# Kernel optimization log

Hardware: AMD Instinct MI355X
Metric: run time of the kernel (lower is better)

Reference implementation:

```python
import jax, jax.numpy as jnp
import numpy as np

BN_EPS = 1e-5

def _conv1x1(x, W, b):
    # x: (B,C,H,W), W: (O,C) -> (B,O,H,W)
    return jnp.einsum('oc,bchw->bohw', W, x) + b[None, :, None, None]

def setup_inputs() -> dict:
    key = jax.random.key(0)
    ks = jax.random.split(key, 6)
    B, C, H, W = 4, 256, 64, 64
    cq = C // 8
    x  = jax.random.normal(ks[0], (B, C, H, W), jnp.float32)
    Wq = jax.random.normal(ks[1], (cq, C), jnp.float32) * (1.0 / np.sqrt(C))
    Wk = jax.random.normal(ks[2], (cq, C), jnp.float32) * (1.0 / np.sqrt(C))
    Wv = jax.random.normal(ks[3], (C, C), jnp.float32) * (1.0 / np.sqrt(C))
    Wo = jax.random.normal(ks[4], (C, C, 3, 3), jnp.float32) * (1.0 / np.sqrt(C * 9))
    return {
        'x': x,
        'Wq': Wq, 'bq': jnp.zeros((cq,), jnp.float32),
        'Wk': Wk, 'bk': jnp.zeros((cq,), jnp.float32),
        'Wv': Wv, 'bv': jnp.zeros((C,), jnp.float32),
        'Wo': Wo, 'bo': jnp.zeros((C,), jnp.float32),
        'bn_gamma': jnp.ones((C,), jnp.float32),
        'bn_beta':  jnp.zeros((C,), jnp.float32),
        'bn_mean':  jnp.zeros((C,), jnp.float32),
        'bn_var':   jnp.ones((C,), jnp.float32),
    }

def reference(x, Wq, bq, Wk, bk, Wv, bv, Wo, bo, bn_gamma, bn_beta, bn_mean, bn_var):
    B, C, H, W = x.shape
    cq = Wq.shape[0]
    N = H * W
    q = _conv1x1(x, Wq, bq).reshape(B, cq, N)   # (B,cq,N)
    k = _conv1x1(x, Wk, bk).reshape(B, cq, N)   # (B,cq,N)
    v = _conv1x1(x, Wv, bv).reshape(B, C, N)    # (B,C,N)
    scale = cq ** (-0.5)
    attn = jnp.einsum('bcn,bcm->bnm', q, k) * scale   # (B,N,N)
    attn = jax.nn.softmax(attn, axis=-1)
    out = jnp.einsum('bnm,bcm->bcn', attn, v).reshape(B, C, H, W)
    # conv_output: 3x3 conv + BN (inference stats) + ReLU
    out = jax.lax.conv_general_dilated(
        out, Wo, window_strides=(1, 1), padding=((1, 1), (1, 1)),
        dimension_numbers=('NCHW', 'OIHW', 'NCHW')) + bo[None, :, None, None]
    inv = bn_gamma * jax.lax.rsqrt(bn_var + BN_EPS)
    out = out * inv[None, :, None, None] + (bn_beta - bn_mean * inv)[None, :, None, None]
    out = jax.nn.relu(out)
    return out + x
```

## Files before the change

### kernel.cpp

```cpp
#include <hip/hip_runtime.h>
#include <hip/hip_bf16.h>
#include <math.h>

#define N_TOK 4096

typedef __attribute__((ext_vector_type(8))) short short8;
typedef __attribute__((ext_vector_type(4))) float f32x4;

#define MFMA16(a, b, c) __builtin_amdgcn_mfma_f32_16x16x32_bf16(a, b, c, 0, 0, 0)

__device__ inline unsigned pack_bf16x2(float a, float b) {
    __hip_bfloat16 ha = __float2bfloat16(a), hb = __float2bfloat16(b);
    unsigned short ua = *(unsigned short*)&ha, ub = *(unsigned short*)&hb;
    return (unsigned)ua | ((unsigned)ub << 16);
}

__device__ inline float bf2f(unsigned short u) {
    unsigned v = ((unsigned)u) << 16;
    union { unsigned u; float f; } cv; cv.u = v; return cv.f;
}

__device__ inline int swz4(int h, int row) { return (h ^ row ^ (row >> 2)) & 3; }

#define SCK 0.25506974748975505f

__global__ __launch_bounds__(256) void w_prep_kernel(
    const float* __restrict__ Wo, const float* __restrict__ Wq,
    const float* __restrict__ Wk, const float* __restrict__ Wv,
    __hip_bfloat16* __restrict__ Wt, __hip_bfloat16* __restrict__ Wqk,
    __hip_bfloat16* __restrict__ Wvb)
{
    int blk = blockIdx.x, t = threadIdx.x;
    if (blk < 256) {
        const float* src = &Wo[(size_t)(blk * 256 + t) * 9];
#pragma unroll
        for (int tap = 0; tap < 9; ++tap)
            Wt[(size_t)(tap * 256 + blk) * 256 + t] = __float2bfloat16(src[tap]);
    } else if (blk < 260) {
        int r0 = (blk - 256) * 64;
        for (int r = r0; r < r0 + 64; ++r)
            Wvb[r * 256 + t] = __float2bfloat16(Wv[r * 256 + t]);
    } else {
        for (int r = 0; r < 32; ++r) {
            Wqk[r * 256 + t]        = __float2bfloat16(Wq[r * 256 + t] * SCK);
            Wqk[(r + 32) * 256 + t] = __float2bfloat16(Wk[r * 256 + t]);
        }
    }
}

__global__ __launch_bounds__(256) void qkv_kernel(
    const float* __restrict__ x,
    const __hip_bfloat16* __restrict__ Wqk, const __hip_bfloat16* __restrict__ Wvb,
    const float* __restrict__ bq, const float* __restrict__ bk,
    const float* __restrict__ bv,
    __hip_bfloat16* __restrict__ qg, __hip_bfloat16* __restrict__ kg,
    __hip_bfloat16* __restrict__ vg)
{
    __shared__ __hip_bfloat16 tl[64][72];
    int blk = blockIdx.x;
    int b = blk >> 6, n0 = (blk & 63) * 64;
    int t = threadIdx.x, w = t >> 6, lane = t & 63;
    int l15 = lane & 15, l4 = lane >> 4;
    int n = n0 + w * 16 + l15;

    f32x4 zf = {0.f, 0.f, 0.f, 0.f};
    f32x4 aqk[4], av[16];
#pragma unroll
    for (int m = 0; m < 4; ++m) aqk[m] = zf;
#pragma unroll
    for (int m = 0; m < 16; ++m) av[m] = zf;

    int cr = t >> 4, part = t & 15;

    for (int cc = 0; cc < 256; cc += 64) {
        __syncthreads();
#pragma unroll
        for (int rep = 0; rep < 4; ++rep) {
            int c = rep * 16 + cr;
            float4 v4 = *(const float4*)&x[((size_t)(b * 256 + cc + c)) * N_TOK + n0 + part * 4];
            tl[part * 4 + 0][c] = __float2bfloat16(v4.x);
            tl[part * 4 + 1][c] = __float2bfloat16(v4.y);
            tl[part * 4 + 2][c] = __float2bfloat16(v4.z);
            tl[part * 4 + 3][c] = __float2bfloat16(v4.w);
        }
        __syncthreads();
#pragma unroll
        for (int kk = 0; kk < 2; ++kk) {
            int k0 = cc + kk * 32;
            short8 bfr = *(const short8*)&tl[w * 16 + l15][kk * 32 + l4 * 8];
#pragma unroll
            for (int m = 0; m < 4; ++m) {
                short8 af = *(const short8*)&Wqk[(size_t)(m * 16 + l15) * 256 + k0 + l4 * 8];
                aqk[m] = MFMA16(af, bfr, aqk[m]);
            }
#pragma unroll
            for (int m = 0; m < 16; ++m) {
                short8 af = *(const short8*)&Wvb[(size_t)(m * 16 + l15) * 256 + k0 + l4 * 8];
                av[m] = MFMA16(af, bfr, av[m]);
            }
        }
    }

    f32x4 bq0 = *(const f32x4*)&bq[l4 * 4];
    f32x4 bq1 = *(const f32x4*)&bq[16 + l4 * 4];
    f32x4 bk0 = *(const f32x4*)&bk[l4 * 4];
    f32x4 bk1 = *(const f32x4*)&bk[16 + l4 * 4];
    size_t obase = (size_t)(b * N_TOK + n) * 32;
    uint2 u;
    u.x = pack_bf16x2(aqk[0][0] + bq0[0] * SCK, aqk[0][1] + bq0[1] * SCK);
    u.y = pack_bf16x2(aqk[0][2] + bq0[2] * SCK, aqk[0][3] + bq0[3] * SCK);
    *(uint2*)&qg[obase + l4 * 4] = u;
    u.x = pack_bf16x2(aqk[1][0] + bq1[0] * SCK, aqk[1][1] + bq1[1] * SCK);
    u.y = pack_bf16x2(aqk[1][2] + bq1[2] * SCK, aqk[1][3] + bq1[3] * SCK);
    *(uint2*)&qg[obase + 16 + l4 * 4] = u;
    u.x = pack_bf16x2(aqk[2][0] + bk0[0], aqk[2][1] + bk0[1]);
    u.y = pack_bf16x2(aqk[2][2] + bk0[2], aqk[2][3] + bk0[3]);
    *(uint2*)&kg[obase + l4 * 4] = u;
    u.x = pack_bf16x2(aqk[3][0] + bk1[0], aqk[3][1] + bk1[1]);
    u.y = pack_bf16x2(aqk[3][2] + bk1[2], aqk[3][3] + bk1[3]);
    *(uint2*)&kg[obase + 16 + l4 * 4] = u;

#pragma unroll
    for (int m = 0; m < 16; ++m) {
        int cb = m * 16 + l4 * 4;
        f32x4 bvv = *(const f32x4*)&bv[cb];
#pragma unroll
        for (int r = 0; r < 4; ++r)
            vg[((size_t)(b * 256 + cb + r)) * N_TOK + n] = __float2bfloat16(av[m][r] + bvv[r]);
    }
}

__global__ __launch_bounds__(256, 2) void flash_kernel(
    const __hip_bfloat16* __restrict__ qg, const __hip_bfloat16* __restrict__ kg,
    const __hip_bfloat16* __restrict__ vg,
    __hip_bfloat16* __restrict__ ph0, __hip_bfloat16* __restrict__ ph1,
    float* __restrict__ Lh)
{
    __shared__ __hip_bfloat16 v_lds[2][128 * 64];
    __shared__ __hip_bfloat16 k_lds[2][64 * 32];
    __shared__ __hip_bfloat16 p_lds[4][32 * 64];

    int blk = blockIdx.x;
    int work = (blk & 7) * 64 + (blk >> 3);
    int g = work >> 6;
    int kh = g >> 2, cs = (g >> 1) & 1, bl = g & 1;
    int rem = work & 63;
    int b = ((rem >> 5) << 1) | bl;
    int qgp = rem & 31;
    int t = threadIdx.x, w = t >> 6, lane = t & 63;
    int l15 = lane & 15, l4 = lane >> 4;
    int qw = qgp * 128 + w * 32;

    short8 qf[2];
#pragma unroll
    for (int qs = 0; qs < 2; ++qs)
        qf[qs] = *(const short8*)&qg[((size_t)(b * N_TOK + qw + qs * 16 + l15)) * 32 + l4 * 8];

    f32x4 zf = {0.f, 0.f, 0.f, 0.f};
    f32x4 acc[2][8];
#pragma unroll
    for (int qs = 0; qs < 2; ++qs)
#pragma unroll
        for (int ct = 0; ct < 8; ++ct) acc[qs][ct] = zf;
    float Lr[2] = {0.f, 0.f};

    int vc  = t >> 1;
    int kb4 = (t & 1) * 4;
    int kr  = t >> 2;
    int kch = t & 3;

    const __hip_bfloat16* vrow  = &vg[((size_t)(b * 256 + cs * 128 + vc)) * N_TOK + kh * 2048];
    const __hip_bfloat16* kbase = &kg[((size_t)(b * N_TOK + kh * 2048)) * 32];

    uint4 vp[4], kp;

#pragma unroll
    for (int j = 0; j < 4; ++j)
        vp[j] = *(const uint4*)&vrow[(kb4 + j) * 8];
    kp = *(const uint4*)&kbase[kr * 32 + kch * 8];
#pragma unroll
    for (int j = 0; j < 4; ++j)
        *(uint4*)&v_lds[0][vc * 64 + (((2 * (kb4 + j)) ^ (vc & 14)) << 2)] = vp[j];
    *(uint4*)&k_lds[0][kr * 32 + swz4(kch, kr) * 8] = kp;
    __syncthreads();

    int buf = 0;
    for (int it = 0; it < 32; ++it) {
        int nm0 = it * 64 + 64;
        bool more = (it < 31);
        if (more) {
#pragma unroll
            for (int j = 0; j < 4; ++j)
                vp[j] = *(const uint4*)&vrow[nm0 + (kb4 + j) * 8];
            kp = *(const uint4*)&kbase[(size_t)(nm0 + kr) * 32 + kch * 8];
        }

        short8 kf[4];
#pragma unroll
        for (int kt = 0; kt < 4; ++kt) {
            int row = kt * 16 + l15;
            kf[kt] = *(const short8*)&k_lds[buf][row * 32 + swz4(l4, row) * 8];
        }
        f32x4 sf[2][4];
#pragma unroll
        for (int qs = 0; qs < 2; ++qs)
#pragma unroll
            for (int kt = 0; kt < 4; ++kt)
                sf[qs][kt] = MFMA16(kf[kt], qf[qs], zf);

#pragma unroll
        for (int qs = 0; qs < 2; ++qs) {
            int prow = qs * 16 + l15;
#pragma unroll
            for (int kt = 0; kt < 4; ++kt) {
                float p0 = exp2f(sf[qs][kt][0]);
                float p1 = exp2f(sf[qs][kt][1]);
                float p2 = exp2f(sf[qs][kt][2]);
                float p3 = exp2f(sf[qs][kt][3]);
                Lr[qs] += (p0 + p1) + (p2 + p3);
                uint2 u;
                u.x = pack_bf16x2(p0, p1);
                u.y = pack_bf16x2(p2, p3);
                *(uint2*)&p_lds[w][prow * 64 + (((kt * 4 + l4) ^ (l15 & 14)) << 2)] = u;
            }
        }

#pragma unroll
        for (int ks = 0; ks < 2; ++ks) {
            short8 pb[2];
#pragma unroll
            for (int qs = 0; qs < 2; ++qs)
                pb[qs] = *(const short8*)&p_lds[w][(qs * 16 + l15) * 64 +
                         (((ks * 8 + l4 * 2) ^ (l15 & 14)) << 2)];
#pragma unroll
            for (int ct = 0; ct < 8; ++ct) {
                int cr = ct * 16 + l15;
                short8 vf = *(const short8*)&v_lds[buf][cr * 64 +
                           (((ks * 8 + l4 * 2) ^ (cr & 14)) << 2)];
                acc[0][ct] = MFMA16(vf, pb[0], acc[0][ct]);
                acc[1][ct] = MFMA16(vf, pb[1], acc[1][ct]);
            }
        }

        if (more) {
#pragma unroll
            for (int j = 0; j < 4; ++j)
                *(uint4*)&v_lds[buf ^ 1][vc * 64 + (((2 * (kb4 + j)) ^ (vc & 14)) << 2)] = vp[j];
            *(uint4*)&k_lds[buf ^ 1][kr * 32 + swz4(kch, kr) * 8] = kp;
            buf ^= 1;
        }
        __syncthreads();
    }

#pragma unroll
    for (int qs = 0; qs < 2; ++qs) {
        float L = Lr[qs];
        L += __shfl_xor(L, 16);
        L += __shfl_xor(L, 32);
        int nq = qw + qs * 16 + l15;
        if (cs == 0 && l4 == 0)
            Lh[kh * 16384 + b * 4096 + nq] = L;
        __hip_bfloat16* pdst = kh ? ph1 : ph0;
        size_t pix = (size_t)(b * N_TOK + nq);
#pragma unroll
        for (int ct = 0; ct < 8; ++ct) {
            int cl = cs * 128 + ct * 16 + l4 * 4;
            uint2 u;
            u.x = pack_bf16x2(acc[qs][ct][0], acc[qs][ct][1]);
            u.y = pack_bf16x2(acc[qs][ct][2], acc[qs][ct][3]);
            *(uint2*)&pdst[pix * 256 + cl] = u;
        }
    }
}

__global__ __launch_bounds__(256) void conv_mfma_kernel(
    const __hip_bfloat16* __restrict__ ph0, const __hip_bfloat16* __restrict__ ph1,
    const float* __restrict__ Lh, const __hip_bfloat16* __restrict__ Wt,
    const float* __restrict__ bo,  const float* __restrict__ gamma,
    const float* __restrict__ beta, const float* __restrict__ mean,
    const float* __restrict__ var, const float* __restrict__ x,
    float* __restrict__ out)
{
    __shared__ __hip_bfloat16 in_lds[180 * 32];
    __shared__ __hip_bfloat16 wt_lds[9 * 64 * 32];

    int blk = blockIdx.x;
    int sp = blk & 31, ob = (blk >> 5) & 3, b = blk >> 7;
    int y0 = (sp >> 2) * 8, x0 = (sp & 3) * 16;
    int o0 = ob * 64;
    int t = threadIdx.x;
    int w = t >> 6, lane = t & 63;
    int l15 = lane & 15, l4 = lane >> 4;

    f32x4 zf = {0.f, 0.f, 0.f, 0.f};
    f32x4 acc[4][2];
#pragma unroll
    for (int m = 0; m < 4; ++m)
#pragma unroll
        for (int n = 0; n < 2; ++n) acc[m][n] = zf;

    for (int cc = 0; cc < 256; cc += 32) {
        __syncthreads();
        for (int jj = t; jj < 720; jj += 256) {
            int pix = jj >> 2, h = jj & 3;
            int iy = pix / 18, ix = pix - iy * 18;
            int gy = y0 - 1 + iy, gx = x0 - 1 + ix;
            uint4 val = {0u, 0u, 0u, 0u};
            if (gy >= 0 && gy < 64 && gx >= 0 && gx < 64) {
                int bn = b * 4096 + gy * 64 + gx;
                float inv = 1.f / (Lh[bn] + Lh[16384 + bn]);
                size_t e = (size_t)bn * 256 + cc + h * 8;
                uint4 a  = *(const uint4*)&ph0[e];
                uint4 b4 = *(const uint4*)&ph1[e];
                const unsigned* ap = (const unsigned*)&a;
                const unsigned* bp = (const unsigned*)&b4;
                unsigned* vpn = (unsigned*)&val;
#pragma unroll
                for (int j = 0; j < 4; ++j) {
                    float lo = (bf2f((unsigned short)(ap[j] & 0xffff)) +
                                bf2f((unsigned short)(bp[j] & 0xffff))) * inv;
                    float hi = (bf2f((unsigned short)(ap[j] >> 16)) +
                                bf2f((unsigned short)(bp[j] >> 16))) * inv;
                    vpn[j] = pack_bf16x2(lo, hi);
                }
            }
            *(uint4*)&in_lds[pix * 32 + swz4(h, pix) * 8] = val;
        }
        for (int jj = t; jj < 2304; jj += 256) {
            int tap = jj >> 8, rem = jj & 255;
            int o = rem >> 2, h = rem & 3;
            uint4 wv = *(const uint4*)&Wt[((size_t)(tap * 256 + o0 + o)) * 256 + cc + h * 8];
            *(uint4*)&wt_lds[tap * 2048 + o * 32 + swz4(h, o) * 8] = wv;
        }
        __syncthreads();

#pragma unroll
        for (int ky = 0; ky < 3; ++ky) {
#pragma unroll
            for (int kx = 0; kx < 3; ++kx) {
                int tap = ky * 3 + kx;
                short8 af[4];
#pragma unroll
                for (int m = 0; m < 4; ++m) {
                    int orow = m * 16 + l15;
                    af[m] = *(const short8*)&wt_lds[tap * 2048 + orow * 32 + swz4(l4, orow) * 8];
                }
#pragma unroll
                for (int ntw = 0; ntw < 2; ++ntw) {
                    int yy = w * 2 + ntw;
                    int p = (yy + ky) * 18 + kx + l15;
                    short8 bfr = *(const short8*)&in_lds[p * 32 + swz4(l4, p) * 8];
#pragma unroll
                    for (int m = 0; m < 4; ++m)
                        acc[m][ntw] = MFMA16(af[m], bfr, acc[m][ntw]);
                }
            }
        }
    }

#pragma unroll
    for (int m = 0; m < 4; ++m) {
#pragma unroll
        for (int r = 0; r < 4; ++r) {
            int oc = o0 + m * 16 + l4 * 4 + r;
            float inv = gamma[oc] * rsqrtf(var[oc] + 1e-5f);
            float sh  = (bo[oc] - mean[oc]) * inv + beta[oc];
#pragma unroll
            for (int ntw = 0; ntw < 2; ++ntw) {
                int gy = y0 + w * 2 + ntw, gx = x0 + l15;
                size_t idx = (size_t)(b * 256 + oc) * 4096 + (size_t)gy * 64 + gx;
                float yv = acc[m][ntw][r] * inv + sh;
                yv = fmaxf(yv, 0.f);
                out[idx] = yv + x[idx];
            }
        }
    }
}

extern "C" void kernel_launch(void* const* d_in, const int* in_sizes, int n_in,
                              void* d_out, int out_size, void* d_ws, size_t ws_size,
                              hipStream_t stream)
{
    const float* x  = (const float*)d_in[0];
    const float* Wq = (const float*)d_in[1];
    const float* bq = (const float*)d_in[2];
    const float* Wk = (const float*)d_in[3];
    const float* bk = (const float*)d_in[4];
    const float* Wv = (const float*)d_in[5];
    const float* bv = (const float*)d_in[6];
    const float* Wo = (const float*)d_in[7];
    const float* bo = (const float*)d_in[8];
    const float* gm = (const float*)d_in[9];
    const float* bt = (const float*)d_in[10];
    const float* mn = (const float*)d_in[11];
    const float* vr = (const float*)d_in[12];
    float* out = (float*)d_out;

    char* wsb = (char*)d_ws;
    __hip_bfloat16* qg  = (__hip_bfloat16*)(wsb);
    __hip_bfloat16* kg  = (__hip_bfloat16*)(wsb + (1u  << 20));
    __hip_bfloat16* vg  = (__hip_bfloat16*)(wsb + (2u  << 20));
    __hip_bfloat16* ph1 = (__hip_bfloat16*)(wsb + (10u << 20));
    __hip_bfloat16* Wt  = (__hip_bfloat16*)(wsb + (18u << 20));
    __hip_bfloat16* ph0 = (__hip_bfloat16*)(wsb + (20u << 20));
    __hip_bfloat16* Wqk = (__hip_bfloat16*)(wsb + (28u << 20));
    __hip_bfloat16* Wvb = (__hip_bfloat16*)(wsb + (28u << 20) + 65536);
    float*          Lh  = (float*)(wsb + (28u << 20) + 262144);

    w_prep_kernel  <<<261,  256, 0, stream>>>(Wo, Wq, Wk, Wv, Wt, Wqk, Wvb);
    qkv_kernel     <<<256,  256, 0, stream>>>(x, Wqk, Wvb, bq, bk, bv, qg, kg, vg);
    flash_kernel   <<<512,  256, 0, stream>>>(qg, kg, vg, ph0, ph1, Lh);
    conv_mfma_kernel<<<512, 256, 0, stream>>>(ph0, ph1, Lh, Wt, bo, gm, bt, mn, vr, x, out);
}
```

Measured before the change: 155.2 us.

## Split QKV projection across waves by output rows and double grid size

The QKV projection kernel now processes 32 tokens per block instead of 64 and launches 512 blocks. Each wave pair splits the 320 output rows into two groups of 10 MFMA tiles, which cuts per-wave accumulator registers from 20 tiles to 10 and doubles block-level parallelism. The flash kernel loop is also unrolled by 2 so the double-buffer index becomes a compile-time value. The trade-off is that the x tile is loaded and converted once per 32 tokens, so weight reads from cache are repeated across twice as many blocks.

New measurement: 187.5 us. 20.8% more time.

```diff
diff --git a/kernel.cpp b/kernel.cpp
--- a/kernel.cpp
+++ b/kernel.cpp
@@ -56,77 +56,90 @@
     __hip_bfloat16* __restrict__ qg, __hip_bfloat16* __restrict__ kg,
     __hip_bfloat16* __restrict__ vg)
 {
-    __shared__ __hip_bfloat16 tl[64][72];
+    __shared__ __hip_bfloat16 tl[32][72];
     int blk = blockIdx.x;
-    int b = blk >> 6, n0 = (blk & 63) * 64;
+    int b = blk >> 7, n0 = (blk & 127) * 32;
     int t = threadIdx.x, w = t >> 6, lane = t & 63;
     int l15 = lane & 15, l4 = lane >> 4;
-    int n = n0 + w * 16 + l15;
+    int ns = w & 1, mg = w >> 1;
+    int n = n0 + ns * 16 + l15;
+
+    const __hip_bfloat16* wrow[10];
+#pragma unroll
+    for (int mi = 0; mi < 10; ++mi) {
+        int row = mg ? ((6 + mi) * 16 + l15)
+                     : (mi < 4 ? (mi * 16 + l15) : 0);
+        const __hip_bfloat16* base = mg ? Wvb : (mi < 4 ? Wqk : Wvb);
+        if (!mg && mi >= 4) row = (mi - 4) * 16 + l15;
+        wrow[mi] = &base[(size_t)row * 256];
+    }
 
     f32x4 zf = {0.f, 0.f, 0.f, 0.f};
-    f32x4 aqk[4], av[16];
-#pragma unroll
-    for (int m = 0; m < 4; ++m) aqk[m] = zf;
-#pragma unroll
-    for (int m = 0; m < 16; ++m) av[m] = zf;
-
-    int cr = t >> 4, part = t & 15;
+    f32x4 acc[10];
+#pragma unroll
+    for (int m = 0; m < 10; ++m) acc[m] = zf;
 
     for (int cc = 0; cc < 256; cc += 64) {
         __syncthreads();
 #pragma unroll
-        for (int rep = 0; rep < 4; ++rep) {
-            int c = rep * 16 + cr;
-            float4 v4 = *(const float4*)&x[((size_t)(b * 256 + cc + c)) * N_TOK + n0 + part * 4];
-            tl[part * 4 + 0][c] = __float2bfloat16(v4.x);
-            tl[part * 4 + 1][c] = __float2bfloat16(v4.y);
-            tl[part * 4 + 2][c] = __float2bfloat16(v4.z);
-            tl[part * 4 + 3][c] = __float2bfloat16(v4.w);
+        for (int rep = 0; rep < 2; ++rep) {
+            int c = rep * 32 + (t >> 3);
+            int n4 = (t & 7) * 4;
+            float4 v4 = *(const float4*)&x[((size_t)(b * 256 + cc + c)) * N_TOK + n0 + n4];
+            tl[n4 + 0][c] = __float2bfloat16(v4.x);
+            tl[n4 + 1][c] = __float2bfloat16(v4.y);
+            tl[n4 + 2][c] = __float2bfloat16(v4.z);
+            tl[n4 + 3][c] = __float2bfloat16(v4.w);
         }
         __syncthreads();
 #pragma unroll
         for (int kk = 0; kk < 2; ++kk) {
             int k0 = cc + kk * 32;
-            short8 bfr = *(const short8*)&tl[w * 16 + l15][kk * 32 + l4 * 8];
-#pragma unroll
-            for (int m = 0; m < 4; ++m) {
-                short8 af = *(const short8*)&Wqk[(size_t)(m * 16 + l15) * 256 + k0 + l4 * 8];
-                aqk[m] = MFMA16(af, bfr, aqk[m]);
-            }
-#pragma unroll
-            for (int m = 0; m < 16; ++m) {
-                short8 af = *(const short8*)&Wvb[(size_t)(m * 16 + l15) * 256 + k0 + l4 * 8];
-                av[m] = MFMA16(af, bfr, av[m]);
-            }
-        }
-    }
-
-    f32x4 bq0 = *(const f32x4*)&bq[l4 * 4];
-    f32x4 bq1 = *(const f32x4*)&bq[16 + l4 * 4];
-    f32x4 bk0 = *(const f32x4*)&bk[l4 * 4];
-    f32x4 bk1 = *(const f32x4*)&bk[16 + l4 * 4];
-    size_t obase = (size_t)(b * N_TOK + n) * 32;
-    uint2 u;
-    u.x = pack_bf16x2(aqk[0][0] + bq0[0] * SCK, aqk[0][1] + bq0[1] * SCK);
-    u.y = pack_bf16x2(aqk[0][2] + bq0[2] * SCK, aqk[0][3] + bq0[3] * SCK);
-    *(uint2*)&qg[obase + l4 * 4] = u;
-    u.x = pack_bf16x2(aqk[1][0] + bq1[0] * SCK, aqk[1][1] + bq1[1] * SCK);
-    u.y = pack_bf16x2(aqk[1][2] + bq1[2] * SCK, aqk[1][3] + bq1[3] * SCK);
-    *(uint2*)&qg[obase + 16 + l4 * 4] = u;
-    u.x = pack_bf16x2(aqk[2][0] + bk0[0], aqk[2][1] + bk0[1]);
-    u.y = pack_bf16x2(aqk[2][2] + bk0[2], aqk[2][3] + bk0[3]);
-    *(uint2*)&kg[obase + l4 * 4] = u;
-    u.x = pack_bf16x2(aqk[3][0] + bk1[0], aqk[3][1] + bk1[1]);
-    u.y = pack_bf16x2(aqk[3][2] + bk1[2], aqk[3][3] + bk1[3]);
-    *(uint2*)&kg[obase + 16 + l4 * 4] = u;
-
-#pragma unroll
-    for (int m = 0; m < 16; ++m) {
-        int cb = m * 16 + l4 * 4;
-        f32x4 bvv = *(const f32x4*)&bv[cb];
-#pragma unroll
-        for (int r = 0; r < 4; ++r)
-            vg[((size_t)(b * 256 + cb + r)) * N_TOK + n] = __float2bfloat16(av[m][r] + bvv[r]);
+            short8 bfr = *(const short8*)&tl[ns * 16 + l15][kk * 32 + l4 * 8];
+#pragma unroll
+            for (int mi = 0; mi < 10; ++mi) {
+                short8 af = *(const short8*)&wrow[mi][k0 + l4 * 8];
+                acc[mi] = MFMA16(af, bfr, acc[mi]);
+            }
+        }
+    }
+
+    if (mg == 0) {
+        f32x4 bq0 = *(const f32x4*)&bq[l4 * 4];
+        f32x4 bq1 = *(const f32x4*)&bq[16 + l4 * 4];
+        f32x4 bk0 = *(const f32x4*)&bk[l4 * 4];
+        f32x4 bk1 = *(const f32x4*)&bk[16 + l4 * 4];
+        size_t obase = (size_t)(b * N_TOK + n) * 32;
+        uint2 u;
+        u.x = pack_bf16x2(acc[0][0] + bq0[0] * SCK, acc[0][1] + bq0[1] * SCK);
+        u.y = pack_bf16x2(acc[0][2] + bq0[2] * SCK, acc[0][3] + bq0[3] * SCK);
+        *(uint2*)&qg[obase + l4 * 4] = u;
+        u.x = pack_bf16x2(acc[1][0] + bq1[0] * SCK, acc[1][1] + bq1[1] * SCK);
+        u.y = pack_bf16x2(acc[1][2] + bq1[2] * SCK, acc[1][3] + bq1[3] * SCK);
+        *(uint2*)&qg[obase + 16 + l4 * 4] = u;
+        u.x = pack_bf16x2(acc[2][0] + bk0[0], acc[2][1] + bk0[1]);
+        u.y = pack_bf16x2(acc[2][2] + bk0[2], acc[2][3] + bk0[3]);
+        *(uint2*)&kg[obase + l4 * 4] = u;
+        u.x = pack_bf16x2(acc[3][0] + bk1[0], acc[3][1] + bk1[1]);
+        u.y = pack_bf16x2(acc[3][2] + bk1[2], acc[3][3] + bk1[3]);
+        *(uint2*)&kg[obase + 16 + l4 * 4] = u;
+#pragma unroll
+        for (int mi = 4; mi < 10; ++mi) {
+            int cb = (mi - 4) * 16 + l4 * 4;
+            f32x4 bvv = *(const f32x4*)&bv[cb];
+#pragma unroll
+            for (int r = 0; r < 4; ++r)
+                vg[((size_t)(b * 256 + cb + r)) * N_TOK + n] = __float2bfloat16(acc[mi][r] + bvv[r]);
+        }
+    } else {
+#pragma unroll
+        for (int mi = 0; mi < 10; ++mi) {
+            int cb = (6 + mi) * 16 + l4 * 4;
+            f32x4 bvv = *(const f32x4*)&bv[cb];
+#pragma unroll
+            for (int r = 0; r < 4; ++r)
+                vg[((size_t)(b * 256 + cb + r)) * N_TOK + n] = __float2bfloat16(acc[mi][r] + bvv[r]);
+        }
     }
 }
 
@@ -184,8 +197,9 @@
     *(uint4*)&k_lds[0][kr * 32 + swz4(kch, kr) * 8] = kp;
     __syncthreads();
 
-    int buf = 0;
+#pragma unroll 2
     for (int it = 0; it < 32; ++it) {
+        const int buf = it & 1;
         int nm0 = it * 64 + 64;
         bool more = (it < 31);
         if (more) {
@@ -247,7 +261,6 @@
             for (int j = 0; j < 4; ++j)
                 *(uint4*)&v_lds[buf ^ 1][vc * 64 + (((2 * (kb4 + j)) ^ (vc & 14)) << 2)] = vp[j];
             *(uint4*)&k_lds[buf ^ 1][kr * 32 + swz4(kch, kr) * 8] = kp;
-            buf ^= 1;
         }
         __syncthreads();
     }
@@ -408,7 +421,7 @@
     float*          Lh  = (float*)(wsb + (28u << 20) + 262144);
 
     w_prep_kernel  <<<261,  256, 0, stream>>>(Wo, Wq, Wk, Wv, Wt, Wqk, Wvb);
-    qkv_kernel     <<<256,  256, 0, stream>>>(x, Wqk, Wvb, bq, bk, bv, qg, kg, vg);
+    qkv_kernel     <<<512,  256, 0, stream>>>(x, Wqk, Wvb, bq, bk, bv, qg, kg, vg);
     flash_kernel   <<<512,  256, 0, stream>>>(qg, kg, vg, ph0, ph1, Lh);
     conv_mfma_kernel<<<512, 256, 0, stream>>>(ph0, ph1, Lh, Wt, bo, gm, bt, mn, vr, x, out);
 }
```
